# Performance work log

Hardware: AMD Instinct MI355X
Metric: run time of the kernel (lower is better)

## Reference

```python
import jax, jax.numpy as jnp
import numpy as np

C = 128
Y_ANCHORS = 16
X_ANCHORS = 16
H = 256
W = 256


def _cubic(t):
    # PyTorch bicubic convolution kernel, a = -0.75
    a = -0.75
    at = jnp.abs(t)
    near = ((a + 2.0) * at - (a + 3.0)) * at * at + 1.0
    far = (((at - 5.0) * at + 8.0) * at - 4.0) * a
    return jnp.where(at <= 1.0, near, jnp.where(at < 2.0, far, 0.0))


def _bicubic_weight_matrix(out_size, in_size):
    # Row-stochastic (out_size, in_size) matrix replicating torch
    # F.interpolate(mode='bicubic', align_corners=False) with index clamping.
    scale = in_size / out_size
    src = (jnp.arange(out_size, dtype=jnp.float32) + 0.5) * scale - 0.5
    i0 = jnp.floor(src)
    t = src - i0
    offs = jnp.arange(-1, 3)
    w = _cubic(t[:, None] - offs[None, :].astype(jnp.float32))  # (out, 4)
    idx = jnp.clip(i0[:, None].astype(jnp.int32) + offs[None, :], 0, in_size - 1)
    Wm = jnp.zeros((out_size, in_size), jnp.float32)
    return Wm.at[jnp.arange(out_size)[:, None], idx].add(w)


def setup_inputs() -> dict:
    key = jax.random.key(0)
    k1, k2, k3 = jax.random.split(key, 3)
    x = jax.random.normal(k1, (2, C, H, W), jnp.float32)
    mean_table = jax.random.normal(k2, (Y_ANCHORS, X_ANCHORS, C), jnp.float32)
    # stds from previously processed tiles are positive; shift rand away from 0
    std_table = jax.random.uniform(k3, (Y_ANCHORS, X_ANCHORS, C), jnp.float32) + 0.5
    weight = jnp.ones((1, C, 1, 1), jnp.float32)
    bias = jnp.zeros((1, C, 1, 1), jnp.float32)
    return {
        'x': x, 'mean_table': mean_table, 'std_table': std_table,
        'weight': weight, 'bias': bias,
        'y_anchor': 4, 'x_anchor': 5, 'pre_y1_anchor': 5, 'pre_x1_anchor': 6,
    }


def reference(x, mean_table, std_table, weight, bias,
              y_anchor, x_anchor, pre_y1_anchor, pre_x1_anchor):
    real_x, pre_x = jnp.split(x, 2, axis=0)  # each (1,C,H,W)
    h, w = real_x.shape[2], real_x.shape[3]
    n = h * w

    # --- prefetched tile: unbiased instance-norm stats, written into the tables
    pre_mean = jnp.mean(pre_x, axis=(2, 3))  # (1,C)
    pre_var = jnp.sum((pre_x - pre_mean[:, :, None, None]) ** 2, axis=(2, 3)) / (n - 1)
    pre_std = jnp.sqrt(pre_var)  # (1,C), torch.std_mean default unbiased
    mean_table = mean_table.at[pre_y1_anchor, pre_x1_anchor].set(pre_mean[0])
    std_table = std_table.at[pre_y1_anchor, pre_x1_anchor].set(pre_std[0])

    # --- replication pad (left=1,right=2,top=1,bottom=2) -> (Y+3, X+3, C)
    pm = jnp.pad(mean_table, ((1, 2), (1, 2), (0, 0)), mode='edge')
    ps = jnp.pad(std_table, ((1, 2), (1, 2), (0, 0)), mode='edge')

    # --- 4x4 anchor window around the current tile
    mean_patch = jax.lax.dynamic_slice(pm, (y_anchor, x_anchor, 0), (4, 4, C))
    std_patch = jax.lax.dynamic_slice(ps, (y_anchor, x_anchor, 0), (4, 4, C))

    # --- bicubic 4x4 -> (3h,3w), center-crop to (h,w); crop folded into weights
    Wy = _bicubic_weight_matrix(3 * h, 4)[h // 2:h // 2 + h]  # (h,4)
    Wx = _bicubic_weight_matrix(3 * w, 4)[w // 2:w // 2 + w]  # (w,4)
    mean_map = jnp.einsum('oy,yxc,px->cop', Wy, mean_patch, Wx)[None]        # (1,C,h,w)
    stdinv_map = jnp.einsum('oy,yxc,px->cop', Wy, 1.0 / std_patch, Wx)[None]  # (1,C,h,w)

    real = (real_x - mean_map) * stdinv_map * weight + bias
    pre = (pre_x - pre_mean[:, :, None, None]) / pre_std[:, :, None, None] * weight + bias
    return jnp.concatenate([real, pre], axis=0)
```

## Files before the change

### kernel.cpp

```cpp
#include <hip/hip_runtime.h>
#include <hip/hip_bf16.h>

#define C 128
#define H 256
#define W 256
#define HW (H * W)
#define CHW (C * H * W)
#define NTAB 16

__device__ __forceinline__ float cubic075(float u) {
    float au = fabsf(u);
    float near_ = (1.25f * au - 2.25f) * au * au + 1.0f;
    float far_  = -0.75f * (((au - 5.0f) * au + 8.0f) * au - 4.0f);
    return au <= 1.0f ? near_ : (au < 2.0f ? far_ : 0.0f);
}

__device__ __forceinline__ void bicubic_w4(int o, float* w4) {
    const float scale = 4.0f / 768.0f;
    float src = ((float)(o + 128) + 0.5f) * scale - 0.5f;
    float i0f = floorf(src);
    float t = src - i0f;
    int i0 = (int)i0f;
    w4[0] = w4[1] = w4[2] = w4[3] = 0.0f;
#pragma unroll
    for (int j = 0; j < 4; ++j) {
        int off = j - 1;
        float wv = cubic075(t - (float)off);
        int idx = i0 + off;
        idx = idx < 0 ? 0 : (idx > 3 ? 3 : idx);
        w4[idx] += wv;
    }
}

__global__ __launch_bounds__(256) void stats_kernel(const float* __restrict__ x,
                                                    float* __restrict__ ws) {
    int c = blockIdx.x >> 3;
    int seg = blockIdx.x & 7;
    const float4* x4 = (const float4*)(x + CHW) + (size_t)c * (HW / 4) + seg * 2048;
    float s = 0.0f, s2 = 0.0f;
#pragma unroll
    for (int k = 0; k < 8; ++k) {
        float4 v = x4[k * 256 + threadIdx.x];
        s  += v.x + v.y + v.z + v.w;
        s2 += v.x * v.x + v.y * v.y + v.z * v.z + v.w * v.w;
    }
#pragma unroll
    for (int off = 32; off > 0; off >>= 1) {
        s  += __shfl_down(s, off);
        s2 += __shfl_down(s2, off);
    }
    __shared__ float sd[8];
    int wid = threadIdx.x >> 6;
    if ((threadIdx.x & 63) == 0) { sd[wid] = s; sd[4 + wid] = s2; }
    __syncthreads();
    if (threadIdx.x == 0) {
        float ts  = sd[0] + sd[1] + sd[2] + sd[3];
        float ts2 = sd[4] + sd[5] + sd[6] + sd[7];
        atomicAdd(&ws[c], ts);
        atomicAdd(&ws[C + c], ts2);
    }
}

__global__ __launch_bounds__(128) void finalize_kernel(
    const float* __restrict__ mean_table, const float* __restrict__ std_table,
    const float* __restrict__ weight, const float* __restrict__ bias,
    const int* __restrict__ yA, const int* __restrict__ xA,
    const int* __restrict__ pyA, const int* __restrict__ pxA,
    float* __restrict__ ws) {
    int c = threadIdx.x;
    const float n = (float)HW;
    float sum = ws[c], sumsq = ws[C + c];
    float mean = sum / n;
    float var = (sumsq - sum * sum / n) / (n - 1.0f);
    float stdv = sqrtf(var);
    float wgt = weight[c], bs = bias[c];
    float sp = wgt / stdv;
    ws[2 * C + c] = sp;
    ws[3 * C + c] = bs - mean * sp;

    int ya = *yA, xa = *xA, py = *pyA, px = *pxA;
    ya = min(max(ya, 0), 19 - 4);
    xa = min(max(xa, 0), 19 - 4);
    float* meanPatch = ws + 4 * C;
    float* invPatch  = ws + 20 * C;
#pragma unroll
    for (int dy = 0; dy < 4; ++dy) {
        int row = min(max(ya + dy - 1, 0), NTAB - 1);
#pragma unroll
        for (int dx = 0; dx < 4; ++dx) {
            int col = min(max(xa + dx - 1, 0), NTAB - 1);
            float m, s;
            if (row == py && col == px) { m = mean; s = stdv; }
            else {
                m = mean_table[(row * NTAB + col) * C + c];
                s = std_table[(row * NTAB + col) * C + c];
            }
            meanPatch[(dy * 4 + dx) * C + c] = m;
            invPatch[(dy * 4 + dx) * C + c] = 1.0f / s;
        }
    }
}

__global__ __launch_bounds__(256) void main_kernel(const float* __restrict__ x,
                                                   const float* __restrict__ weight,
                                                   const float* __restrict__ bias,
                                                   const float* __restrict__ ws,
                                                   float* __restrict__ out) {
    int b = blockIdx.x;
    if (b < 1024) {
        int o = b & 255;
        int g = b >> 8;
        int p = threadIdx.x;
        float wy[4], wx[4];
        bicubic_w4(o, wy);
        bicubic_w4(p, wx);
        const float* meanPatch = ws + 4 * C;
        const float* invPatch  = ws + 20 * C;
        __shared__ float Am[4 * 32];
        __shared__ float Ai[4 * 32];
        {
            int t = threadIdx.x;
            int xx = (t & 127) >> 5;
            int cc = t & 31;
            int c = g * 32 + cc;
            const float* src = (t < 128) ? meanPatch : invPatch;
            float a = 0.0f;
#pragma unroll
            for (int y = 0; y < 4; ++y) a += wy[y] * src[(y * 4 + xx) * C + c];
            if (t < 128) Am[xx * 32 + cc] = a;
            else         Ai[xx * 32 + cc] = a;
        }
        __syncthreads();
        const float* xrow = x + o * W + p;
        float* orow = out + o * W + p;
        for (int cc = 0; cc < 32; ++cc) {
            int c = g * 32 + cc;
            float m = 0.0f, iv = 0.0f;
#pragma unroll
            for (int xx = 0; xx < 4; ++xx) {
                m  += wx[xx] * Am[xx * 32 + cc];
                iv += wx[xx] * Ai[xx * 32 + cc];
            }
            float xv = xrow[(size_t)c * HW];
            orow[(size_t)c * HW] = (xv - m) * iv * weight[c] + bias[c];
        }
    } else {
        int bb = b - 1024;
        const float4* xin = (const float4*)(x + CHW);
        float4* outp = (float4*)(out + CHW);
        const float* scaleP = ws + 2 * C;
        const float* biasP  = ws + 3 * C;
        int i = bb * 256 + threadIdx.x;
#pragma unroll
        for (int k = 0; k < 8; ++k) {
            int j = i + k * 262144;
            float4 v = xin[j];
            int c = j >> 14;
            float sp = scaleP[c], bp = biasP[c];
            float4 r;
            r.x = v.x * sp + bp;
            r.y = v.y * sp + bp;
            r.z = v.z * sp + bp;
            r.w = v.w * sp + bp;
            outp[j] = r;
        }
    }
}

extern "C" void kernel_launch(void* const* d_in, const int* in_sizes, int n_in,
                              void* d_out, int out_size, void* d_ws, size_t ws_size,
                              hipStream_t stream) {
    const float* x          = (const float*)d_in[0];
    const float* mean_table = (const float*)d_in[1];
    const float* std_table  = (const float*)d_in[2];
    const float* weight     = (const float*)d_in[3];
    const float* bias       = (const float*)d_in[4];
    const int* yA  = (const int*)d_in[5];
    const int* xA  = (const int*)d_in[6];
    const int* pyA = (const int*)d_in[7];
    const int* pxA = (const int*)d_in[8];
    float* out = (float*)d_out;
    float* ws  = (float*)d_ws;

    hipMemsetAsync(ws, 0, 2 * C * sizeof(float), stream);
    stats_kernel<<<C * 8, 256, 0, stream>>>(x, ws);
    finalize_kernel<<<1, 128, 0, stream>>>(mean_table, std_table, weight, bias,
                                           yA, xA, pyA, pxA, ws);
    main_kernel<<<2048, 256, 0, stream>>>(x, weight, bias, ws, out);
}
```

Before: 141.6 us.

## Fold finalize into main kernel, drop memset and atomics, vectorize real-branch loads

Stats blocks now write per-segment partial sums instead of atomically accumulating, which removes the memset and atomics. The single-block finalize kernel is gone: each main-kernel block recomputes channel statistics and builds its anchor patch in shared memory. The real-tile branch now loads and stores float4, with each thread handling four columns and one wave per eight channels. The cost is redundant per-block stats and patch work, plus extra shared-memory use.

Result: faster. 137.7 us (-2.7%).

```diff
diff --git a/kernel.cpp b/kernel.cpp
--- a/kernel.cpp
+++ b/kernel.cpp
@@ -54,109 +54,123 @@
     if ((threadIdx.x & 63) == 0) { sd[wid] = s; sd[4 + wid] = s2; }
     __syncthreads();
     if (threadIdx.x == 0) {
-        float ts  = sd[0] + sd[1] + sd[2] + sd[3];
-        float ts2 = sd[4] + sd[5] + sd[6] + sd[7];
-        atomicAdd(&ws[c], ts);
-        atomicAdd(&ws[C + c], ts2);
-    }
-}
-
-__global__ __launch_bounds__(128) void finalize_kernel(
+        ws[c * 8 + seg]        = sd[0] + sd[1] + sd[2] + sd[3];
+        ws[1024 + c * 8 + seg] = sd[4] + sd[5] + sd[6] + sd[7];
+    }
+}
+
+__device__ __forceinline__ void channel_stats(const float* __restrict__ ws, int c,
+                                              float& mean, float& stdv) {
+    float s = 0.0f, s2 = 0.0f;
+#pragma unroll
+    for (int k = 0; k < 8; ++k) { s += ws[c * 8 + k]; s2 += ws[1024 + c * 8 + k]; }
+    const float n = (float)HW;
+    mean = s / n;
+    float var = (s2 - s * s / n) / (n - 1.0f);
+    stdv = sqrtf(var);
+}
+
+__global__ __launch_bounds__(256) void main_kernel(
+    const float* __restrict__ x,
     const float* __restrict__ mean_table, const float* __restrict__ std_table,
     const float* __restrict__ weight, const float* __restrict__ bias,
     const int* __restrict__ yA, const int* __restrict__ xA,
     const int* __restrict__ pyA, const int* __restrict__ pxA,
-    float* __restrict__ ws) {
-    int c = threadIdx.x;
-    const float n = (float)HW;
-    float sum = ws[c], sumsq = ws[C + c];
-    float mean = sum / n;
-    float var = (sumsq - sum * sum / n) / (n - 1.0f);
-    float stdv = sqrtf(var);
-    float wgt = weight[c], bs = bias[c];
-    float sp = wgt / stdv;
-    ws[2 * C + c] = sp;
-    ws[3 * C + c] = bs - mean * sp;
-
-    int ya = *yA, xa = *xA, py = *pyA, px = *pxA;
-    ya = min(max(ya, 0), 19 - 4);
-    xa = min(max(xa, 0), 19 - 4);
-    float* meanPatch = ws + 4 * C;
-    float* invPatch  = ws + 20 * C;
-#pragma unroll
-    for (int dy = 0; dy < 4; ++dy) {
-        int row = min(max(ya + dy - 1, 0), NTAB - 1);
-#pragma unroll
-        for (int dx = 0; dx < 4; ++dx) {
-            int col = min(max(xa + dx - 1, 0), NTAB - 1);
-            float m, s;
-            if (row == py && col == px) { m = mean; s = stdv; }
-            else {
-                m = mean_table[(row * NTAB + col) * C + c];
-                s = std_table[(row * NTAB + col) * C + c];
-            }
-            meanPatch[(dy * 4 + dx) * C + c] = m;
-            invPatch[(dy * 4 + dx) * C + c] = 1.0f / s;
-        }
-    }
-}
-
-__global__ __launch_bounds__(256) void main_kernel(const float* __restrict__ x,
-                                                   const float* __restrict__ weight,
-                                                   const float* __restrict__ bias,
-                                                   const float* __restrict__ ws,
-                                                   float* __restrict__ out) {
+    const float* __restrict__ ws, float* __restrict__ out) {
     int b = blockIdx.x;
+    int t = threadIdx.x;
     if (b < 1024) {
         int o = b & 255;
         int g = b >> 8;
-        int p = threadIdx.x;
-        float wy[4], wx[4];
+        __shared__ float patchM[16 * 32];
+        __shared__ float patchI[16 * 32];
+        __shared__ float Am[4 * 32], Ai[4 * 32], Wgt[32], Bs[32];
+        {
+            int cc = t & 31;
+            int e0 = t >> 5;
+            int c = g * 32 + cc;
+            float mean, stdv;
+            channel_stats(ws, c, mean, stdv);
+            int ya = min(max(*yA, 0), 15);
+            int xa = min(max(*xA, 0), 15);
+            int py = *pyA, px = *pxA;
+#pragma unroll
+            for (int e = e0; e < 16; e += 8) {
+                int row = min(max(ya + (e >> 2) - 1, 0), NTAB - 1);
+                int col = min(max(xa + (e & 3) - 1, 0), NTAB - 1);
+                float m, s;
+                if (row == py && col == px) { m = mean; s = stdv; }
+                else {
+                    m = mean_table[(row * NTAB + col) * C + c];
+                    s = std_table[(row * NTAB + col) * C + c];
+                }
+                patchM[e * 32 + cc] = m;
+                patchI[e * 32 + cc] = 1.0f / s;
+            }
+            if (e0 == 0) { Wgt[cc] = weight[c]; Bs[cc] = bias[c]; }
+        }
+        __syncthreads();
+        float wy[4];
         bicubic_w4(o, wy);
-        bicubic_w4(p, wx);
-        const float* meanPatch = ws + 4 * C;
-        const float* invPatch  = ws + 20 * C;
-        __shared__ float Am[4 * 32];
-        __shared__ float Ai[4 * 32];
         {
-            int t = threadIdx.x;
-            int xx = (t & 127) >> 5;
+            int xx = (t >> 5) & 3;
             int cc = t & 31;
-            int c = g * 32 + cc;
-            const float* src = (t < 128) ? meanPatch : invPatch;
+            const float* src = (t < 128) ? patchM : patchI;
             float a = 0.0f;
 #pragma unroll
-            for (int y = 0; y < 4; ++y) a += wy[y] * src[(y * 4 + xx) * C + c];
+            for (int y = 0; y < 4; ++y) a += wy[y] * src[(y * 4 + xx) * 32 + cc];
             if (t < 128) Am[xx * 32 + cc] = a;
             else         Ai[xx * 32 + cc] = a;
         }
         __syncthreads();
-        const float* xrow = x + o * W + p;
-        float* orow = out + o * W + p;
-        for (int cc = 0; cc < 32; ++cc) {
+
+        int w = t >> 6, l = t & 63;
+        float wx[4][4];
+#pragma unroll
+        for (int e = 0; e < 4; ++e) bicubic_w4(4 * l + e, wx[e]);
+        const float4* xin = (const float4*)x;
+        float4* outp = (float4*)out;
+#pragma unroll
+        for (int k = 0; k < 8; ++k) {
+            int cc = w * 8 + k;
             int c = g * 32 + cc;
-            float m = 0.0f, iv = 0.0f;
-#pragma unroll
-            for (int xx = 0; xx < 4; ++xx) {
-                m  += wx[xx] * Am[xx * 32 + cc];
-                iv += wx[xx] * Ai[xx * 32 + cc];
+            size_t base = ((size_t)c * HW + o * W) / 4 + l;
+            float4 v = xin[base];
+            float wgt = Wgt[cc], bsv = Bs[cc];
+            float r[4], vv[4] = {v.x, v.y, v.z, v.w};
+#pragma unroll
+            for (int e = 0; e < 4; ++e) {
+                float m = 0.0f, iv = 0.0f;
+#pragma unroll
+                for (int xx = 0; xx < 4; ++xx) {
+                    m  += wx[e][xx] * Am[xx * 32 + cc];
+                    iv += wx[e][xx] * Ai[xx * 32 + cc];
+                }
+                r[e] = (vv[e] - m) * iv * wgt + bsv;
             }
-            float xv = xrow[(size_t)c * HW];
-            orow[(size_t)c * HW] = (xv - m) * iv * weight[c] + bias[c];
+            float4 ro = {r[0], r[1], r[2], r[3]};
+            outp[base] = ro;
         }
     } else {
         int bb = b - 1024;
+        __shared__ float Sp[C], Bp[C];
+        if (t < C) {
+            float mean, stdv;
+            channel_stats(ws, t, mean, stdv);
+            float sp = weight[t] / stdv;
+            Sp[t] = sp;
+            Bp[t] = bias[t] - mean * sp;
+        }
+        __syncthreads();
         const float4* xin = (const float4*)(x + CHW);
         float4* outp = (float4*)(out + CHW);
-        const float* scaleP = ws + 2 * C;
-        const float* biasP  = ws + 3 * C;
-        int i = bb * 256 + threadIdx.x;
+        int i = bb * 256 + t;
 #pragma unroll
         for (int k = 0; k < 8; ++k) {
             int j = i + k * 262144;
             float4 v = xin[j];
             int c = j >> 14;
-            float sp = scaleP[c], bp = biasP[c];
+            float sp = Sp[c], bp = Bp[c];
             float4 r;
             r.x = v.x * sp + bp;
             r.y = v.y * sp + bp;
@@ -182,9 +196,7 @@
     float* out = (float*)d_out;
     float* ws  = (float*)d_ws;
 
-    hipMemsetAsync(ws, 0, 2 * C * sizeof(float), stream);
     stats_kernel<<<C * 8, 256, 0, stream>>>(x, ws);
-    finalize_kernel<<<1, 128, 0, stream>>>(mean_table, std_table, weight, bias,
-                                           yA, xA, pyA, pxA, ws);
-    main_kernel<<<2048, 256, 0, stream>>>(x, weight, bias, ws, out);
-}
+    main_kernel<<<2048, 256, 0, stream>>>(x, mean_table, std_table, weight, bias,
+                                          yA, xA, pyA, pxA, ws, out);
+}
```
